# Kernel tuning notes

Measured on AMD Instinct MI355X. Metric: run time of the kernel, lower is better.

Reference implementation:

```python
import jax, jax.numpy as jnp
import numpy as np

CUTOFF = 2.0
LOG2 = float(np.log(2.0))

def ssp(x):
    # shifted softplus: softplus(x) - log(2)
    return jax.nn.softplus(x) - LOG2

def setup_inputs() -> dict:
    key = jax.random.key(0)
    ks = jax.random.split(key, 12)
    N, E, H, F, G = 10000, 320000, 256, 256, 50
    x = jax.random.normal(ks[0], (N, H), dtype=jnp.float32)
    edge_index = jax.random.randint(ks[1], (2, E), 0, N, dtype=jnp.int64)
    edge_weight = jax.random.normal(ks[2], (E, 3), dtype=jnp.float32)
    edge_attr = jax.random.normal(ks[3], (E, G), dtype=jnp.float32)
    s = lambda fan_in: 1.0 / np.sqrt(fan_in)
    mlp_w1 = jax.random.uniform(ks[4], (G, F), jnp.float32, -s(G), s(G))
    mlp_b1 = jax.random.uniform(ks[5], (F,), jnp.float32, -s(G), s(G))
    mlp_w2 = jax.random.uniform(ks[6], (F, F), jnp.float32, -s(F), s(F))
    mlp_b2 = jax.random.uniform(ks[7], (F,), jnp.float32, -s(F), s(F))
    lin1_w = jax.random.uniform(ks[8], (H, F), jnp.float32, -s(H), s(H))
    lin2_w = jax.random.uniform(ks[9], (F, H), jnp.float32, -s(F), s(F))
    lin2_b = jax.random.uniform(ks[10], (H,), jnp.float32, -s(F), s(F))
    return {"x": x, "edge_index": edge_index, "edge_weight": edge_weight,
            "edge_attr": edge_attr, "mlp_w1": mlp_w1, "mlp_b1": mlp_b1,
            "mlp_w2": mlp_w2, "mlp_b2": mlp_b2, "lin1_w": lin1_w,
            "lin2_w": lin2_w, "lin2_b": lin2_b}

def reference(x, edge_index, edge_weight, edge_attr,
              mlp_w1, mlp_b1, mlp_w2, mlp_b2, lin1_w, lin2_w, lin2_b):
    N = x.shape[0]
    # cutoff envelope on edge distances
    distances = jnp.linalg.norm(edge_weight, axis=1)                 # [E]
    C = 0.5 * (jnp.cos(distances * jnp.pi / CUTOFF) + 1.0)
    C = C * (distances <= CUTOFF)                                    # [E]
    # edge filter MLP
    W = ssp(edge_attr @ mlp_w1 + mlp_b1) @ mlp_w2 + mlp_b2           # [E, F]
    W = W * C[:, None]
    i, j = edge_index[0], edge_index[1]
    messages = W * (x[j] @ lin1_w)                                   # [E, F]
    agg = jax.ops.segment_sum(messages, i, num_segments=N)           # [N, F]
    h = ssp(agg @ lin2_w + lin2_b)                                   # [N, H]
    return x + h
```

## Files before the change

kernel.cpp:

```cpp
#include <hip/hip_runtime.h>
#include <hip/hip_bf16.h>
#include <stdint.h>

#define HF 256
#define GG 50

typedef __attribute__((ext_vector_type(8))) short bf16x8;
typedef __attribute__((ext_vector_type(4))) short bf16x4;
typedef __attribute__((ext_vector_type(4))) float f32x4;
typedef float f32x4a __attribute__((ext_vector_type(4), aligned(4)));

__device__ __forceinline__ uint32_t f2bf2u(float a, float b){
    __hip_bfloat162 h = __float22bfloat162_rn(make_float2(a, b));
    union { __hip_bfloat162 h; uint32_t u; } v; v.h = h; return v.u;
}
__device__ __forceinline__ float bf2f(short s){
    union { uint32_t u; float f; } v; v.u = ((uint32_t)(uint16_t)s) << 16;
    return v.f;
}
__device__ __forceinline__ float ssp_f(float x){
    float e = __builtin_amdgcn_exp2f(x * 1.44269504088896341f);
    return 0.69314718055994531f * __builtin_amdgcn_logf(1.0f + e)
         - 0.69314718055994531f;
}

__device__ __forceinline__ void pack_natural(const float* __restrict__ B,
                                             short* __restrict__ Bp,
                                             int idx, int KT, int kmax)
{
    int lane = idx & 63;
    int kt   = (idx >> 6) & (KT - 1);
    int ntg  = idx >> (6 + (KT == 2 ? 1 : 3));
    int col  = ntg * 16 + (lane & 15);
    int k0   = kt * 32 + (lane >> 4) * 8;
    uint32_t u[4];
#pragma unroll
    for (int jj = 0; jj < 4; ++jj) {
        int ka = k0 + 2*jj, kb = ka + 1;
        float a = (ka < kmax) ? B[(size_t)ka * HF + col] : 0.f;
        float b = (kb < kmax) ? B[(size_t)kb * HF + col] : 0.f;
        u[jj] = f2bf2u(a, b);
    }
    *(uint4*)&Bp[(size_t)idx * 8] = *(uint4*)u;
}

__global__ __launch_bounds__(256)
void prep_kernel(const float* __restrict__ w1, const float* __restrict__ b1,
                 const float* __restrict__ w2,
                 const float* __restrict__ lin1, const float* __restrict__ lin2,
                 short* __restrict__ w1p, short* __restrict__ w2p,
                 short* __restrict__ lin1p, short* __restrict__ lin2p,
                 const float* __restrict__ x, short* __restrict__ x_bf, int nx8,
                 const int* __restrict__ eidx, int* __restrict__ cnt, int E,
                 float* __restrict__ agg, int nAgg4, int gConv, int gHist)
{
    int b = blockIdx.x, tid = threadIdx.x;
    if (b < 8) {
        int idx  = b * 256 + tid;
        int lane = idx & 63;
        int kt   = (idx >> 6) & 1;
        int ntg  = idx >> 7;
        int col  = ntg * 16 + (lane & 15);
        int k0   = kt * 32 + (lane >> 4) * 8;
        uint32_t u[4];
#pragma unroll
        for (int jj = 0; jj < 4; ++jj) {
            int ka = k0 + 2*jj, kb = ka + 1;
            float va = (ka < GG) ? w1[(size_t)ka * HF + col]
                                 : ((ka == GG) ? b1[col] : 0.f);
            float vb = (kb < GG) ? w1[(size_t)kb * HF + col]
                                 : ((kb == GG) ? b1[col] : 0.f);
            u[jj] = f2bf2u(va, vb);
        }
        *(uint4*)&w1p[(size_t)idx * 8] = *(uint4*)u;
    } else if (b < 40) {
        int idx = (b - 8) * 256 + tid;
        int lane = idx & 63;
        int kt   = (idx >> 6) & 7;
        int ntg  = idx >> 9;
        int col  = ntg * 16 + (lane & 15);
        int s0   = kt * 32 + (lane >> 4) * 8;
        uint32_t u[4];
#pragma unroll
        for (int jj = 0; jj < 4; ++jj) {
            int sa = s0 + 2*jj, sb = sa + 1;
            int fa = (sa >> 6) * 64 + (sa & 3) * 16 + ((sa & 63) >> 2);
            int fb = (sb >> 6) * 64 + (sb & 3) * 16 + ((sb & 63) >> 2);
            u[jj] = f2bf2u(w2[(size_t)fa * HF + col], w2[(size_t)fb * HF + col]);
        }
        *(uint4*)&w2p[(size_t)idx * 8] = *(uint4*)u;
    } else if (b < 72) {
        pack_natural(lin1, lin1p, (b - 40) * 256 + tid, 8, HF);
    } else if (b < 104) {
        pack_natural(lin2, lin2p, (b - 72) * 256 + tid, 8, HF);
    } else if (b < 104 + gConv) {
        int idx = (b - 104) * 256 + tid;
        if (idx < nx8) {
            const float* xp = x + (size_t)idx * 8;
            float4 p0 = *(const float4*)(xp);
            float4 p1 = *(const float4*)(xp + 4);
            uint32_t u[4] = { f2bf2u(p0.x, p0.y), f2bf2u(p0.z, p0.w),
                              f2bf2u(p1.x, p1.y), f2bf2u(p1.z, p1.w) };
            *(uint4*)&x_bf[(size_t)idx * 8] = *(uint4*)u;
        }
    } else if (b < 104 + gConv + gHist) {
        int e = (b - 104 - gConv) * 256 + tid;
        if (e < E) atomicAdd(&cnt[eidx[e]], 1);
    } else {
        int idx = (b - 104 - gConv - gHist) * 256 + tid;
        if (idx < nAgg4) ((float4*)agg)[idx] = make_float4(0.f, 0.f, 0.f, 0.f);
    }
}

__global__ __launch_bounds__(256)
void gemm_scan_kernel(const short* __restrict__ x_bf, const short* __restrict__ lin1p,
                      short* __restrict__ y_p, int N,
                      const int* __restrict__ cnt, int* __restrict__ row,
                      int* __restrict__ cursor, int E, int gNode)
{
    const int tid = threadIdx.x;
    if ((int)blockIdx.x >= gNode) {
        __shared__ int part[256];
        const int CH = (N + 255) / 256;
        int lo = tid * CH;
        int hi = min(lo + CH, N);
        int s = 0;
        for (int n = lo; n < hi; ++n) s += cnt[n];
        part[tid] = s;
        __syncthreads();
        for (int off = 1; off < 256; off <<= 1) {
            int v = (tid >= off) ? part[tid - off] : 0;
            __syncthreads();
            part[tid] += v;
            __syncthreads();
        }
        int acc = part[tid] - s;
        for (int n = lo; n < hi; ++n) {
            row[n] = acc; cursor[n] = acc;
            acc += cnt[n];
        }
        if (tid == 255) row[N] = E;
        return;
    }
    const int lane = tid & 63;
    const int w    = tid >> 6;
    const int l15  = lane & 15;
    const int quad = lane >> 4;
    const int row0 = blockIdx.x * 32;

    f32x4 acc[2][4];
#pragma unroll
    for (int mt = 0; mt < 2; ++mt)
#pragma unroll
        for (int nt = 0; nt < 4; ++nt) acc[mt][nt] = (f32x4){0.f,0.f,0.f,0.f};

#pragma unroll 2
    for (int kt = 0; kt < 8; ++kt) {
        bf16x8 af[2];
#pragma unroll
        for (int mt = 0; mt < 2; ++mt) {
            int r = row0 + mt * 16 + l15;
            int rl = (r < N) ? r : 0;
            af[mt] = *(const bf16x8*)&x_bf[(size_t)rl * HF + kt * 32 + quad * 8];
        }
#pragma unroll
        for (int nt = 0; nt < 4; ++nt) {
            bf16x8 bfr = *(const bf16x8*)&lin1p[(size_t)(((w*4+nt)*8+kt)*64+lane)*8];
#pragma unroll
            for (int mt = 0; mt < 2; ++mt)
                acc[mt][nt] = __builtin_amdgcn_mfma_f32_16x16x32_bf16(af[mt], bfr, acc[mt][nt], 0, 0, 0);
        }
    }
#pragma unroll
    for (int mt = 0; mt < 2; ++mt) {
#pragma unroll
        for (int r = 0; r < 4; ++r) {
            int row_ = row0 + mt * 16 + quad * 4 + r;
            if (row_ < N) {
                uint2 u = make_uint2(f2bf2u(acc[mt][0][r], acc[mt][1][r]),
                                     f2bf2u(acc[mt][2][r], acc[mt][3][r]));
                *(uint2*)&y_p[(size_t)row_ * HF + w * 64 + l15 * 4] = u;
            }
        }
    }
}

__global__ __launch_bounds__(256)
void scatter_kernel(const int* __restrict__ eidx, int* __restrict__ cursor,
                    int* __restrict__ perm, int E)
{
    int e = blockIdx.x * 256 + threadIdx.x;
    if (e < E) {
        int pos = atomicAdd(&cursor[eidx[e]], 1);
        perm[pos] = e;
    }
}

__global__ __launch_bounds__(256)
void node2_kernel(const float* __restrict__ agg, const short* __restrict__ lin2p,
                  const float* __restrict__ bias, const float* __restrict__ x,
                  float* __restrict__ out, int N)
{
    const int tid  = threadIdx.x;
    const int lane = tid & 63;
    const int w    = tid >> 6;
    const int l15  = lane & 15;
    const int quad = lane >> 4;
    const int row0 = blockIdx.x * 32;

    f32x4 acc[2][4];
#pragma unroll
    for (int mt = 0; mt < 2; ++mt)
#pragma unroll
        for (int nt = 0; nt < 4; ++nt) acc[mt][nt] = (f32x4){0.f,0.f,0.f,0.f};

#pragma unroll 2
    for (int kt = 0; kt < 8; ++kt) {
        bf16x8 af[2];
#pragma unroll
        for (int mt = 0; mt < 2; ++mt) {
            int r = row0 + mt * 16 + l15;
            int rl = (r < N) ? r : 0;
            const float* ap = agg + (size_t)rl * HF + kt * 32 + quad * 8;
            float4 p0 = *(const float4*)(ap);
            float4 p1 = *(const float4*)(ap + 4);
            union { uint32_t u[4]; bf16x8 v; } c;
            c.u[0] = f2bf2u(p0.x, p0.y); c.u[1] = f2bf2u(p0.z, p0.w);
            c.u[2] = f2bf2u(p1.x, p1.y); c.u[3] = f2bf2u(p1.z, p1.w);
            af[mt] = c.v;
        }
#pragma unroll
        for (int nt = 0; nt < 4; ++nt) {
            bf16x8 bfr = *(const bf16x8*)&lin2p[(size_t)(((w*4+nt)*8+kt)*64+lane)*8];
#pragma unroll
            for (int mt = 0; mt < 2; ++mt)
                acc[mt][nt] = __builtin_amdgcn_mfma_f32_16x16x32_bf16(af[mt], bfr, acc[mt][nt], 0, 0, 0);
        }
    }
    float bs[4];
#pragma unroll
    for (int nt = 0; nt < 4; ++nt) bs[nt] = bias[w * 64 + nt * 16 + l15];
#pragma unroll
    for (int mt = 0; mt < 2; ++mt) {
#pragma unroll
        for (int r = 0; r < 4; ++r) {
            int row_ = row0 + mt * 16 + quad * 4 + r;
            if (row_ < N) {
#pragma unroll
                for (int nt = 0; nt < 4; ++nt) {
                    int f = w * 64 + nt * 16 + l15;
                    float v = ssp_f(acc[mt][nt][r] + bs[nt]) + x[(size_t)row_ * HF + f];
                    out[(size_t)row_ * HF + f] = v;
                }
            }
        }
    }
}

__global__ __launch_bounds__(256, 3)
void edge_mfma(const float* __restrict__ ea, const int* __restrict__ eidx,
               const float* __restrict__ ew,
               const short* __restrict__ w1p,
               const short* __restrict__ w2p, const float* __restrict__ b2,
               const short* __restrict__ y_p, const int* __restrict__ perm,
               const int* __restrict__ rowp,
               float* __restrict__ agg, int E)
{
    __shared__ short smem[19584];
    short* hid  = smem;
    short* msgT = smem;
    short* St   = smem + 18432;
    __shared__ int s_runnode[64];
    __shared__ unsigned char s_runcomp[64];

    const int tid  = threadIdx.x;
    const int lane = tid & 63;
    const int w    = tid >> 6;
    const int l15  = lane & 15;
    const int quad = lane >> 4;
    const int e0   = blockIdx.x * 64;

    int pp = e0 + lane;
    int eL = 0, iv = -1;
    float c = 0.f;
    if (pp < E) {
        eL = perm[pp];
        iv = eidx[eL];
        float d0 = ew[eL*3+0], d1 = ew[eL*3+1], d2 = ew[eL*3+2];
        float d = sqrtf(d0*d0 + d1*d1 + d2*d2);
        c = (d <= 2.0f) ? 0.5f * (__cosf(d * 1.57079632679489662f) + 1.0f) : 0.f;
    }
    int jv = eidx[E + eL];
    int ivn = __shfl_down(iv, 1);
    bool flag = (lane == 63) || (iv != ivn);
    unsigned long long bm = __ballot(flag);
    const int runcnt = (int)__popcll(bm);
    if (w == 0 && flag) {
        int rid = (int)__popcll(bm & ((1ull << lane) - 1ull));
        s_runnode[rid] = iv;
        int comp = 0;
        if (iv >= 0) {
            int lo = rowp[iv], hi = rowp[iv + 1];
            comp = (lo >= e0 && hi <= e0 + 64) ? 1 : 0;
        }
        s_runcomp[rid] = (unsigned char)comp;
    }

    bf16x8 a1[4][2];
#pragma unroll
    for (int mt = 0; mt < 4; ++mt) {
        int rp = __shfl(eL, mt * 16 + l15);
        const float* er = ea + (size_t)rp * GG;
        f32x4a p0 = *(const f32x4a*)(er + quad * 8);
        f32x4a p1 = *(const f32x4a*)(er + quad * 8 + 4);
        union { uint32_t u[4]; bf16x8 v; } ca;
        ca.u[0] = f2bf2u(p0[0], p0[1]); ca.u[1] = f2bf2u(p0[2], p0[3]);
        ca.u[2] = f2bf2u(p1[0], p1[1]); ca.u[3] = f2bf2u(p1[2], p1[3]);
        a1[mt][0] = ca.v;
        union { uint32_t u[4]; bf16x8 v; } cb;
        if (quad < 2) {
            f32x4a q0 = *(const f32x4a*)(er + 32 + quad * 8);
            f32x4a q1 = *(const f32x4a*)(er + 36 + quad * 8);
            cb.u[0] = f2bf2u(q0[0], q0[1]); cb.u[1] = f2bf2u(q0[2], q0[3]);
            cb.u[2] = f2bf2u(q1[0], q1[1]); cb.u[3] = f2bf2u(q1[2], q1[3]);
        } else if (quad == 2) {
            float2 q = *(const float2*)(er + 48);
            cb.u[0] = f2bf2u(q.x, q.y);
            cb.u[1] = 0x00003F80u;
            cb.u[2] = 0u; cb.u[3] = 0u;
        } else {
            cb.u[0] = 0u; cb.u[1] = 0u; cb.u[2] = 0u; cb.u[3] = 0u;
        }
        a1[mt][1] = cb.v;
    }

    f32x4 acc1[4][4];
#pragma unroll
    for (int mt = 0; mt < 4; ++mt)
#pragma unroll
        for (int nt = 0; nt < 4; ++nt) acc1[mt][nt] = (f32x4){0.f,0.f,0.f,0.f};
#pragma unroll
    for (int kt = 0; kt < 2; ++kt) {
#pragma unroll
        for (int nt = 0; nt < 4; ++nt) {
            bf16x8 bfr = *(const bf16x8*)&w1p[(size_t)(((w*4+nt)*2+kt)*64+lane)*8];
#pragma unroll
            for (int mt = 0; mt < 4; ++mt)
                acc1[mt][nt] = __builtin_amdgcn_mfma_f32_16x16x32_bf16(a1[mt][kt], bfr, acc1[mt][nt], 0, 0, 0);
        }
    }

    bf16x4 yv[4][4];
#pragma unroll
    for (int mt = 0; mt < 4; ++mt)
#pragma unroll
        for (int r = 0; r < 4; ++r) {
            int j = __shfl(jv, mt * 16 + quad * 4 + r);
            yv[mt][r] = *(const bf16x4*)&y_p[(size_t)j * HF + w * 64 + l15 * 4];
        }

#pragma unroll
    for (int mt = 0; mt < 4; ++mt) {
#pragma unroll
        for (int r = 0; r < 4; ++r) {
            int e = mt * 16 + quad * 4 + r;
            float v0 = ssp_f(acc1[mt][0][r]);
            float v1 = ssp_f(acc1[mt][1][r]);
            float v2 = ssp_f(acc1[mt][2][r]);
            float v3 = ssp_f(acc1[mt][3][r]);
            uint2 u = make_uint2(f2bf2u(v0, v1), f2bf2u(v2, v3));
            *(uint2*)&hid[e * 264 + w * 64 + l15 * 4] = u;
        }
    }
    __syncthreads();

    f32x4 acc2[4][4];
#pragma unroll
    for (int mt = 0; mt < 4; ++mt)
#pragma unroll
        for (int nt = 0; nt < 4; ++nt) acc2[mt][nt] = (f32x4){0.f,0.f,0.f,0.f};

#pragma unroll 2
    for (int kt = 0; kt < 8; ++kt) {
        bf16x8 af[4];
#pragma unroll
        for (int mt = 0; mt < 4; ++mt)
            af[mt] = *(bf16x8*)&hid[(mt * 16 + l15) * 264 + kt * 32 + quad * 8];
#pragma unroll
        for (int nt = 0; nt < 4; ++nt) {
            bf16x8 bfr = *(const bf16x8*)&w2p[(size_t)(((w*4+nt)*8+kt)*64+lane)*8];
#pragma unroll
            for (int mt = 0; mt < 4; ++mt)
                acc2[mt][nt] = __builtin_amdgcn_mfma_f32_16x16x32_bf16(af[mt], bfr, acc2[mt][nt], 0, 0, 0);
        }
    }
    __syncthreads();

    float bias2[4];
#pragma unroll
    for (int nt = 0; nt < 4; ++nt) bias2[nt] = b2[w * 64 + nt * 16 + l15];
    float cs[4][4];
#pragma unroll
    for (int mt = 0; mt < 4; ++mt)
#pragma unroll
        for (int r = 0; r < 4; ++r)
            cs[mt][r] = __shfl(c, mt * 16 + quad * 4 + r);
#pragma unroll
    for (int mt = 0; mt < 4; ++mt) {
#pragma unroll
        for (int nt = 0; nt < 4; ++nt) {
            int col = w * 64 + nt * 16 + l15;
            float v0 = (acc2[mt][nt][0] + bias2[nt]) * cs[mt][0] * bf2f(yv[mt][0][nt]);
            float v1 = (acc2[mt][nt][1] + bias2[nt]) * cs[mt][1] * bf2f(yv[mt][1][nt]);
            float v2 = (acc2[mt][nt][2] + bias2[nt]) * cs[mt][2] * bf2f(yv[mt][2][nt]);
            float v3 = (acc2[mt][nt][3] + bias2[nt]) * cs[mt][3] * bf2f(yv[mt][3][nt]);
            uint2 u = make_uint2(f2bf2u(v0, v1), f2bf2u(v2, v3));
            *(uint2*)&msgT[col * 72 + mt * 16 + quad * 4] = u;
        }
    }
    {
        int e   = tid & 63;
        int rb  = tid >> 6;
        int rid = (int)__popcll(bm & ((1ull << e) - 1ull));
#pragma unroll
        for (int q = 0; q < 4; ++q) {
            int r = rb + q * 4;
            St[r * 72 + e] = (rid == r) ? (short)0x3F80 : (short)0;
        }
    }
    __syncthreads();

    for (int ntg = 0; ntg * 16 < runcnt; ++ntg) {
        if (ntg > 0) {
            __syncthreads();
            int e   = tid & 63;
            int rb  = tid >> 6;
            int rid = (int)__popcll(bm & ((1ull << e) - 1ull));
#pragma unroll
            for (int q = 0; q < 4; ++q) {
                int r = rb + q * 4;
                St[r * 72 + e] = (rid == ntg * 16 + r) ? (short)0x3F80 : (short)0;
            }
            __syncthreads();
        }
        f32x4 acc3[4];
#pragma unroll
        for (int mt = 0; mt < 4; ++mt) acc3[mt] = (f32x4){0.f,0.f,0.f,0.f};
#pragma unroll
        for (int kt = 0; kt < 2; ++kt) {
            bf16x8 bS = *(bf16x8*)&St[l15 * 72 + kt * 32 + quad * 8];
#pragma unroll
            for (int mt = 0; mt < 4; ++mt) {
                bf16x8 af = *(bf16x8*)&msgT[(w*64 + mt*16 + l15) * 72 + kt*32 + quad*8];
                acc3[mt] = __builtin_amdgcn_mfma_f32_16x16x32_bf16(af, bS, acc3[mt], 0, 0, 0);
            }
        }
        int r = ntg * 16 + l15;
        if (r < runcnt) {
            int node = s_runnode[r];
            if (node >= 0) {
                float* ap = agg + (size_t)node * HF + w * 64 + quad * 4;
                if (s_runcomp[r]) {
#pragma unroll
                    for (int mt = 0; mt < 4; ++mt) {
                        float4 v = make_float4(acc3[mt][0], acc3[mt][1], acc3[mt][2], acc3[mt][3]);
                        *(float4*)(ap + mt * 16) = v;
                    }
                } else {
#pragma unroll
                    for (int mt = 0; mt < 4; ++mt)
#pragma unroll
                        for (int g = 0; g < 4; ++g)
                            atomicAdd(ap + mt * 16 + g, acc3[mt][g]);
                }
            }
        }
    }
}

extern "C" void kernel_launch(void* const* d_in, const int* in_sizes, int n_in,
                              void* d_out, int out_size, void* d_ws, size_t ws_size,
                              hipStream_t stream)
{
    const float* x     = (const float*)d_in[0];
    const int*   eidx  = (const int*)  d_in[1];
    const float* ew    = (const float*)d_in[2];
    const float* ea    = (const float*)d_in[3];
    const float* w1    = (const float*)d_in[4];
    const float* b1    = (const float*)d_in[5];
    const float* w2    = (const float*)d_in[6];
    const float* b2    = (const float*)d_in[7];
    const float* lin1  = (const float*)d_in[8];
    const float* lin2  = (const float*)d_in[9];
    const float* lin2b = (const float*)d_in[10];
    float* out = (float*)d_out;

    const int N = in_sizes[0] / HF;
    const int E = in_sizes[2] / 3;

    const size_t fN = (size_t)N * HF;
    float* agg    = (float*)d_ws;
    short* y_p    = (short*)(agg + fN);
    short* x_bf   = y_p + fN;
    int*   cnt    = (int*)(x_bf + fN);
    int*   row    = cnt + N;
    int*   cursor = row + (N + 8);
    int*   perm   = cursor + N;
    short* w1p    = (short*)(((uintptr_t)(perm + E) + 255) & ~(uintptr_t)255);
    short* w2p    = w1p + 16384;
    short* lin1p  = w2p + 65536;
    short* lin2p  = lin1p + 65536;

    hipMemsetAsync(cnt, 0, (size_t)N * sizeof(int), stream);

    const int nx8   = (int)(fN / 8);
    const int nAgg4 = (int)(fN / 4);
    const int gConv = (nx8 + 255) / 256;
    const int gHist = (E + 255) / 256;
    const int gZero = (nAgg4 + 255) / 256;
    prep_kernel<<<dim3(104 + gConv + gHist + gZero), dim3(256), 0, stream>>>(
        w1, b1, w2, lin1, lin2, w1p, w2p, lin1p, lin2p, x, x_bf, nx8,
        eidx, cnt, E, agg, nAgg4, gConv, gHist);

    const int gNode = (N + 31) / 32;
    gemm_scan_kernel<<<dim3(gNode + 1), dim3(256), 0, stream>>>(
        x_bf, lin1p, y_p, N, cnt, row, cursor, E, gNode);

    const int gScatter = (E + 255) / 256;
    scatter_kernel<<<dim3(gScatter), dim3(256), 0, stream>>>(eidx, cursor, perm, E);

    edge_mfma<<<dim3((E + 63) / 64), dim3(256), 0, stream>>>(
        ea, eidx, ew, w1p, w2p, b2, y_p, perm, row, agg, E);

    node2_kernel<<<dim3(gNode), dim3(256), 0, stream>>>(
        agg, lin2p, lin2b, x, out, N);
}
```

Measured before the change: 357.3 us.

## Make edge kernel persistent with register-resident weights and prefetch of next tile

Turns edge_mfma into a persistent grid-stride kernel capped at 1000 blocks. The W1 and W2 B-fragments and the bias are now loaded once into registers instead of being reloaded from global memory for every tile. The next tile's perm, edge index, distance, edge_attr and y gathers are issued during the current tile's compute to hide gather latency. The cost is a large rise in register pressure (w2f alone is 32 bf16x8 values per thread), which may cause spills or cut occupancy below the launch bound of 3, plus an extra barrier per iteration.

```diff
diff --git a/kernel.cpp b/kernel.cpp
--- a/kernel.cpp
+++ b/kernel.cpp
@@ -257,6 +257,65 @@
     }
 }
 
+__device__ __forceinline__ void issue_ea(const float* __restrict__ ea, int eLsrc,
+                                         int l15, int quad,
+                                         f32x4a (&rp0)[4], f32x4a (&rp1)[4],
+                                         f32x4a (&rq0)[4], f32x4a (&rq1)[4])
+{
+#pragma unroll
+    for (int mt = 0; mt < 4; ++mt) {
+        int rp = __shfl(eLsrc, mt * 16 + l15);
+        const float* er = ea + (size_t)rp * GG;
+        rp0[mt] = *(const f32x4a*)(er + quad * 8);
+        rp1[mt] = *(const f32x4a*)(er + quad * 8 + 4);
+        if (quad < 2) {
+            rq0[mt] = *(const f32x4a*)(er + 32 + quad * 8);
+            rq1[mt] = *(const f32x4a*)(er + 36 + quad * 8);
+        } else if (quad == 2) {
+            float2 q = *(const float2*)(er + 48);
+            rq0[mt][0] = q.x; rq0[mt][1] = q.y;
+        }
+    }
+}
+
+__device__ __forceinline__ void cvt_a1(int quad,
+                                       const f32x4a (&rp0)[4], const f32x4a (&rp1)[4],
+                                       const f32x4a (&rq0)[4], const f32x4a (&rq1)[4],
+                                       bf16x8 (&a1)[4][2])
+{
+#pragma unroll
+    for (int mt = 0; mt < 4; ++mt) {
+        union { uint32_t u[4]; bf16x8 v; } ca;
+        ca.u[0] = f2bf2u(rp0[mt][0], rp0[mt][1]); ca.u[1] = f2bf2u(rp0[mt][2], rp0[mt][3]);
+        ca.u[2] = f2bf2u(rp1[mt][0], rp1[mt][1]); ca.u[3] = f2bf2u(rp1[mt][2], rp1[mt][3]);
+        a1[mt][0] = ca.v;
+        union { uint32_t u[4]; bf16x8 v; } cb;
+        if (quad < 2) {
+            cb.u[0] = f2bf2u(rq0[mt][0], rq0[mt][1]); cb.u[1] = f2bf2u(rq0[mt][2], rq0[mt][3]);
+            cb.u[2] = f2bf2u(rq1[mt][0], rq1[mt][1]); cb.u[3] = f2bf2u(rq1[mt][2], rq1[mt][3]);
+        } else if (quad == 2) {
+            cb.u[0] = f2bf2u(rq0[mt][0], rq0[mt][1]);
+            cb.u[1] = 0x00003F80u;
+            cb.u[2] = 0u; cb.u[3] = 0u;
+        } else {
+            cb.u[0] = 0u; cb.u[1] = 0u; cb.u[2] = 0u; cb.u[3] = 0u;
+        }
+        a1[mt][1] = cb.v;
+    }
+}
+
+__device__ __forceinline__ void issue_yv(const short* __restrict__ y_p, int jvsrc,
+                                         int w, int l15, int quad, bf16x4 (&yv)[4][4])
+{
+#pragma unroll
+    for (int mt = 0; mt < 4; ++mt)
+#pragma unroll
+        for (int r = 0; r < 4; ++r) {
+            int j = __shfl(jvsrc, mt * 16 + quad * 4 + r);
+            yv[mt][r] = *(const bf16x4*)&y_p[(size_t)j * HF + w * 64 + l15 * 4];
+        }
+}
+
 __global__ __launch_bounds__(256, 3)
 void edge_mfma(const float* __restrict__ ea, const int* __restrict__ eidx,
                const float* __restrict__ ew,
@@ -264,7 +323,7 @@
                const short* __restrict__ w2p, const float* __restrict__ b2,
                const short* __restrict__ y_p, const int* __restrict__ perm,
                const int* __restrict__ rowp,
-               float* __restrict__ agg, int E)
+               float* __restrict__ agg, int E, int grid64)
 {
     __shared__ short smem[19584];
     short* hid  = smem;
@@ -278,8 +337,24 @@
     const int w    = tid >> 6;
     const int l15  = lane & 15;
     const int quad = lane >> 4;
-    const int e0   = blockIdx.x * 64;
-
+
+    bf16x8 w1f[2][4];
+#pragma unroll
+    for (int kt = 0; kt < 2; ++kt)
+#pragma unroll
+        for (int nt = 0; nt < 4; ++nt)
+            w1f[kt][nt] = *(const bf16x8*)&w1p[(size_t)(((w*4+nt)*2+kt)*64+lane)*8];
+    bf16x8 w2f[8][4];
+#pragma unroll
+    for (int kt = 0; kt < 8; ++kt)
+#pragma unroll
+        for (int nt = 0; nt < 4; ++nt)
+            w2f[kt][nt] = *(const bf16x8*)&w2p[(size_t)(((w*4+nt)*8+kt)*64+lane)*8];
+    float bias2[4];
+#pragma unroll
+    for (int nt = 0; nt < 4; ++nt) bias2[nt] = b2[w * 64 + nt * 16 + l15];
+
+    int e0 = blockIdx.x * 64;
     int pp = e0 + lane;
     int eL = 0, iv = -1;
     float c = 0.f;
@@ -291,190 +366,173 @@
         c = (d <= 2.0f) ? 0.5f * (__cosf(d * 1.57079632679489662f) + 1.0f) : 0.f;
     }
     int jv = eidx[E + eL];
-    int ivn = __shfl_down(iv, 1);
-    bool flag = (lane == 63) || (iv != ivn);
-    unsigned long long bm = __ballot(flag);
-    const int runcnt = (int)__popcll(bm);
-    if (w == 0 && flag) {
-        int rid = (int)__popcll(bm & ((1ull << lane) - 1ull));
-        s_runnode[rid] = iv;
-        int comp = 0;
-        if (iv >= 0) {
-            int lo = rowp[iv], hi = rowp[iv + 1];
-            comp = (lo >= e0 && hi <= e0 + 64) ? 1 : 0;
-        }
-        s_runcomp[rid] = (unsigned char)comp;
-    }
-
-    bf16x8 a1[4][2];
-#pragma unroll
-    for (int mt = 0; mt < 4; ++mt) {
-        int rp = __shfl(eL, mt * 16 + l15);
-        const float* er = ea + (size_t)rp * GG;
-        f32x4a p0 = *(const f32x4a*)(er + quad * 8);
-        f32x4a p1 = *(const f32x4a*)(er + quad * 8 + 4);
-        union { uint32_t u[4]; bf16x8 v; } ca;
-        ca.u[0] = f2bf2u(p0[0], p0[1]); ca.u[1] = f2bf2u(p0[2], p0[3]);
-        ca.u[2] = f2bf2u(p1[0], p1[1]); ca.u[3] = f2bf2u(p1[2], p1[3]);
-        a1[mt][0] = ca.v;
-        union { uint32_t u[4]; bf16x8 v; } cb;
-        if (quad < 2) {
-            f32x4a q0 = *(const f32x4a*)(er + 32 + quad * 8);
-            f32x4a q1 = *(const f32x4a*)(er + 36 + quad * 8);
-            cb.u[0] = f2bf2u(q0[0], q0[1]); cb.u[1] = f2bf2u(q0[2], q0[3]);
-            cb.u[2] = f2bf2u(q1[0], q1[1]); cb.u[3] = f2bf2u(q1[2], q1[3]);
-        } else if (quad == 2) {
-            float2 q = *(const float2*)(er + 48);
-            cb.u[0] = f2bf2u(q.x, q.y);
-            cb.u[1] = 0x00003F80u;
-            cb.u[2] = 0u; cb.u[3] = 0u;
-        } else {
-            cb.u[0] = 0u; cb.u[1] = 0u; cb.u[2] = 0u; cb.u[3] = 0u;
-        }
-        a1[mt][1] = cb.v;
-    }
-
-    f32x4 acc1[4][4];
-#pragma unroll
-    for (int mt = 0; mt < 4; ++mt)
-#pragma unroll
-        for (int nt = 0; nt < 4; ++nt) acc1[mt][nt] = (f32x4){0.f,0.f,0.f,0.f};
-#pragma unroll
-    for (int kt = 0; kt < 2; ++kt) {
-#pragma unroll
-        for (int nt = 0; nt < 4; ++nt) {
-            bf16x8 bfr = *(const bf16x8*)&w1p[(size_t)(((w*4+nt)*2+kt)*64+lane)*8];
-#pragma unroll
-            for (int mt = 0; mt < 4; ++mt)
-                acc1[mt][nt] = __builtin_amdgcn_mfma_f32_16x16x32_bf16(a1[mt][kt], bfr, acc1[mt][nt], 0, 0, 0);
-        }
-    }
-
+    f32x4a rp0[4], rp1[4], rq0[4], rq1[4];
+    issue_ea(ea, eL, l15, quad, rp0, rp1, rq0, rq1);
     bf16x4 yv[4][4];
-#pragma unroll
-    for (int mt = 0; mt < 4; ++mt)
-#pragma unroll
-        for (int r = 0; r < 4; ++r) {
-            int j = __shfl(jv, mt * 16 + quad * 4 + r);
-            yv[mt][r] = *(const bf16x4*)&y_p[(size_t)j * HF + w * 64 + l15 * 4];
-        }
-
-#pragma unroll
-    for (int mt = 0; mt < 4; ++mt) {
-#pragma unroll
-        for (int r = 0; r < 4; ++r) {
-            int e = mt * 16 + quad * 4 + r;
-            float v0 = ssp_f(acc1[mt][0][r]);
-            float v1 = ssp_f(acc1[mt][1][r]);
-            float v2 = ssp_f(acc1[mt][2][r]);
-            float v3 = ssp_f(acc1[mt][3][r]);
-            uint2 u = make_uint2(f2bf2u(v0, v1), f2bf2u(v2, v3));
-            *(uint2*)&hid[e * 264 + w * 64 + l15 * 4] = u;
-        }
-    }
-    __syncthreads();
-
-    f32x4 acc2[4][4];
-#pragma unroll
-    for (int mt = 0; mt < 4; ++mt)
-#pragma unroll
-        for (int nt = 0; nt < 4; ++nt) acc2[mt][nt] = (f32x4){0.f,0.f,0.f,0.f};
-
-#pragma unroll 2
-    for (int kt = 0; kt < 8; ++kt) {
-        bf16x8 af[4];
-#pragma unroll
-        for (int mt = 0; mt < 4; ++mt)
-            af[mt] = *(bf16x8*)&hid[(mt * 16 + l15) * 264 + kt * 32 + quad * 8];
-#pragma unroll
-        for (int nt = 0; nt < 4; ++nt) {
-            bf16x8 bfr = *(const bf16x8*)&w2p[(size_t)(((w*4+nt)*8+kt)*64+lane)*8];
-#pragma unroll
-            for (int mt = 0; mt < 4; ++mt)
-                acc2[mt][nt] = __builtin_amdgcn_mfma_f32_16x16x32_bf16(af[mt], bfr, acc2[mt][nt], 0, 0, 0);
-        }
-    }
-    __syncthreads();
-
-    float bias2[4];
-#pragma unroll
-    for (int nt = 0; nt < 4; ++nt) bias2[nt] = b2[w * 64 + nt * 16 + l15];
-    float cs[4][4];
-#pragma unroll
-    for (int mt = 0; mt < 4; ++mt)
-#pragma unroll
-        for (int r = 0; r < 4; ++r)
-            cs[mt][r] = __shfl(c, mt * 16 + quad * 4 + r);
-#pragma unroll
-    for (int mt = 0; mt < 4; ++mt) {
-#pragma unroll
-        for (int nt = 0; nt < 4; ++nt) {
-            int col = w * 64 + nt * 16 + l15;
-            float v0 = (acc2[mt][nt][0] + bias2[nt]) * cs[mt][0] * bf2f(yv[mt][0][nt]);
-            float v1 = (acc2[mt][nt][1] + bias2[nt]) * cs[mt][1] * bf2f(yv[mt][1][nt]);
-            float v2 = (acc2[mt][nt][2] + bias2[nt]) * cs[mt][2] * bf2f(yv[mt][2][nt]);
-            float v3 = (acc2[mt][nt][3] + bias2[nt]) * cs[mt][3] * bf2f(yv[mt][3][nt]);
-            uint2 u = make_uint2(f2bf2u(v0, v1), f2bf2u(v2, v3));
-            *(uint2*)&msgT[col * 72 + mt * 16 + quad * 4] = u;
-        }
-    }
-    {
-        int e   = tid & 63;
-        int rb  = tid >> 6;
-        int rid = (int)__popcll(bm & ((1ull << e) - 1ull));
-#pragma unroll
-        for (int q = 0; q < 4; ++q) {
-            int r = rb + q * 4;
-            St[r * 72 + e] = (rid == r) ? (short)0x3F80 : (short)0;
-        }
-    }
-    __syncthreads();
-
-    for (int ntg = 0; ntg * 16 < runcnt; ++ntg) {
-        if (ntg > 0) {
-            __syncthreads();
+    issue_yv(y_p, jv, w, l15, quad, yv);
+
+    for (; e0 < E; e0 += grid64) {
+        bf16x8 a1[4][2];
+        cvt_a1(quad, rp0, rp1, rq0, rq1, a1);
+
+        int ivn_ = __shfl_down(iv, 1);
+        bool flag = (lane == 63) || (iv != ivn_);
+        unsigned long long bm = __ballot(flag);
+        const int runcnt = (int)__popcll(bm);
+        if (w == 0 && flag) {
+            int rid = (int)__popcll(bm & ((1ull << lane) - 1ull));
+            s_runnode[rid] = iv;
+            int comp = 0;
+            if (iv >= 0) {
+                int lo = rowp[iv], hi = rowp[iv + 1];
+                comp = (lo >= e0 && hi <= e0 + 64) ? 1 : 0;
+            }
+            s_runcomp[rid] = (unsigned char)comp;
+        }
+        {
             int e   = tid & 63;
             int rb  = tid >> 6;
             int rid = (int)__popcll(bm & ((1ull << e) - 1ull));
 #pragma unroll
             for (int q = 0; q < 4; ++q) {
                 int r = rb + q * 4;
-                St[r * 72 + e] = (rid == ntg * 16 + r) ? (short)0x3F80 : (short)0;
-            }
-            __syncthreads();
-        }
-        f32x4 acc3[4];
-#pragma unroll
-        for (int mt = 0; mt < 4; ++mt) acc3[mt] = (f32x4){0.f,0.f,0.f,0.f};
-#pragma unroll
-        for (int kt = 0; kt < 2; ++kt) {
-            bf16x8 bS = *(bf16x8*)&St[l15 * 72 + kt * 32 + quad * 8];
-#pragma unroll
-            for (int mt = 0; mt < 4; ++mt) {
-                bf16x8 af = *(bf16x8*)&msgT[(w*64 + mt*16 + l15) * 72 + kt*32 + quad*8];
-                acc3[mt] = __builtin_amdgcn_mfma_f32_16x16x32_bf16(af, bS, acc3[mt], 0, 0, 0);
-            }
-        }
-        int r = ntg * 16 + l15;
-        if (r < runcnt) {
-            int node = s_runnode[r];
-            if (node >= 0) {
-                float* ap = agg + (size_t)node * HF + w * 64 + quad * 4;
-                if (s_runcomp[r]) {
-#pragma unroll
-                    for (int mt = 0; mt < 4; ++mt) {
-                        float4 v = make_float4(acc3[mt][0], acc3[mt][1], acc3[mt][2], acc3[mt][3]);
-                        *(float4*)(ap + mt * 16) = v;
+                St[r * 72 + e] = (rid == r) ? (short)0x3F80 : (short)0;
+            }
+        }
+
+        const int e0n = e0 + grid64;
+        const int ppn = e0n + lane;
+        int eLn = (ppn < E) ? perm[ppn] : 0;
+
+        f32x4 acc1[4][4];
+#pragma unroll
+        for (int mt = 0; mt < 4; ++mt)
+#pragma unroll
+            for (int nt = 0; nt < 4; ++nt) acc1[mt][nt] = (f32x4){0.f,0.f,0.f,0.f};
+#pragma unroll
+        for (int kt = 0; kt < 2; ++kt)
+#pragma unroll
+            for (int nt = 0; nt < 4; ++nt)
+#pragma unroll
+                for (int mt = 0; mt < 4; ++mt)
+                    acc1[mt][nt] = __builtin_amdgcn_mfma_f32_16x16x32_bf16(a1[mt][kt], w1f[kt][nt], acc1[mt][nt], 0, 0, 0);
+
+#pragma unroll
+        for (int mt = 0; mt < 4; ++mt) {
+#pragma unroll
+            for (int r = 0; r < 4; ++r) {
+                int e = mt * 16 + quad * 4 + r;
+                float v0 = ssp_f(acc1[mt][0][r]);
+                float v1 = ssp_f(acc1[mt][1][r]);
+                float v2 = ssp_f(acc1[mt][2][r]);
+                float v3 = ssp_f(acc1[mt][3][r]);
+                uint2 u = make_uint2(f2bf2u(v0, v1), f2bf2u(v2, v3));
+                *(uint2*)&hid[e * 264 + w * 64 + l15 * 4] = u;
+            }
+        }
+
+        int ivn = (ppn < E) ? eidx[eLn] : -1;
+        int jvn = eidx[E + eLn];
+        float d0n = ew[eLn*3+0], d1n = ew[eLn*3+1], d2n = ew[eLn*3+2];
+
+        __syncthreads();
+
+        f32x4 acc2[4][4];
+#pragma unroll
+        for (int mt = 0; mt < 4; ++mt)
+#pragma unroll
+            for (int nt = 0; nt < 4; ++nt) acc2[mt][nt] = (f32x4){0.f,0.f,0.f,0.f};
+#pragma unroll
+        for (int kt = 0; kt < 8; ++kt) {
+            bf16x8 af[4];
+#pragma unroll
+            for (int mt = 0; mt < 4; ++mt)
+                af[mt] = *(bf16x8*)&hid[(mt * 16 + l15) * 264 + kt * 32 + quad * 8];
+#pragma unroll
+            for (int nt = 0; nt < 4; ++nt)
+#pragma unroll
+                for (int mt = 0; mt < 4; ++mt)
+                    acc2[mt][nt] = __builtin_amdgcn_mfma_f32_16x16x32_bf16(af[mt], w2f[kt][nt], acc2[mt][nt], 0, 0, 0);
+        }
+        __syncthreads();
+
+        float cs[4][4];
+#pragma unroll
+        for (int mt = 0; mt < 4; ++mt)
+#pragma unroll
+            for (int r = 0; r < 4; ++r)
+                cs[mt][r] = __shfl(c, mt * 16 + quad * 4 + r);
+#pragma unroll
+        for (int mt = 0; mt < 4; ++mt) {
+#pragma unroll
+            for (int nt = 0; nt < 4; ++nt) {
+                int col = w * 64 + nt * 16 + l15;
+                float v0 = (acc2[mt][nt][0] + bias2[nt]) * cs[mt][0] * bf2f(yv[mt][0][nt]);
+                float v1 = (acc2[mt][nt][1] + bias2[nt]) * cs[mt][1] * bf2f(yv[mt][1][nt]);
+                float v2 = (acc2[mt][nt][2] + bias2[nt]) * cs[mt][2] * bf2f(yv[mt][2][nt]);
+                float v3 = (acc2[mt][nt][3] + bias2[nt]) * cs[mt][3] * bf2f(yv[mt][3][nt]);
+                uint2 u = make_uint2(f2bf2u(v0, v1), f2bf2u(v2, v3));
+                *(uint2*)&msgT[col * 72 + mt * 16 + quad * 4] = u;
+            }
+        }
+
+        float dn = sqrtf(d0n*d0n + d1n*d1n + d2n*d2n);
+        float cn = (ppn < E && dn <= 2.0f)
+                 ? 0.5f * (__cosf(dn * 1.57079632679489662f) + 1.0f) : 0.f;
+        issue_yv(y_p, jvn, w, l15, quad, yv);
+
+        for (int ntg = 0; ntg * 16 < runcnt; ++ntg) {
+            if (ntg > 0) {
+                __syncthreads();
+                int e   = tid & 63;
+                int rb  = tid >> 6;
+                int rid = (int)__popcll(bm & ((1ull << e) - 1ull));
+#pragma unroll
+                for (int q = 0; q < 4; ++q) {
+                    int r = rb + q * 4;
+                    St[r * 72 + e] = (rid == ntg * 16 + r) ? (short)0x3F80 : (short)0;
+                }
+                __syncthreads();
+            }
+            f32x4 acc3[4];
+#pragma unroll
+            for (int mt = 0; mt < 4; ++mt) acc3[mt] = (f32x4){0.f,0.f,0.f,0.f};
+#pragma unroll
+            for (int kt = 0; kt < 2; ++kt) {
+                bf16x8 bS = *(bf16x8*)&St[l15 * 72 + kt * 32 + quad * 8];
+#pragma unroll
+                for (int mt = 0; mt < 4; ++mt) {
+                    bf16x8 af = *(bf16x8*)&msgT[(w*64 + mt*16 + l15) * 72 + kt*32 + quad*8];
+                    acc3[mt] = __builtin_amdgcn_mfma_f32_16x16x32_bf16(af, bS, acc3[mt], 0, 0, 0);
+                }
+            }
+            int r = ntg * 16 + l15;
+            if (r < runcnt) {
+                int node = s_runnode[r];
+                if (node >= 0) {
+                    float* ap = agg + (size_t)node * HF + w * 64 + quad * 4;
+                    if (s_runcomp[r]) {
+#pragma unroll
+                        for (int mt = 0; mt < 4; ++mt) {
+                            float4 v = make_float4(acc3[mt][0], acc3[mt][1], acc3[mt][2], acc3[mt][3]);
+                            *(float4*)(ap + mt * 16) = v;
+                        }
+                    } else {
+#pragma unroll
+                        for (int mt = 0; mt < 4; ++mt)
+#pragma unroll
+                            for (int g = 0; g < 4; ++g)
+                                atomicAdd(ap + mt * 16 + g, acc3[mt][g]);
                     }
-                } else {
-#pragma unroll
-                    for (int mt = 0; mt < 4; ++mt)
-#pragma unroll
-                        for (int g = 0; g < 4; ++g)
-                            atomicAdd(ap + mt * 16 + g, acc3[mt][g]);
                 }
             }
         }
+
+        issue_ea(ea, eLn, l15, quad, rp0, rp1, rq0, rq1);
+
+        __syncthreads();
+
+        eL = eLn; iv = ivn; jv = jvn; c = cn;
     }
 }
 
@@ -529,8 +587,10 @@
     const int gScatter = (E + 255) / 256;
     scatter_kernel<<<dim3(gScatter), dim3(256), 0, stream>>>(eidx, cursor, perm, E);
 
-    edge_mfma<<<dim3((E + 63) / 64), dim3(256), 0, stream>>>(
-        ea, eidx, ew, w1p, w2p, b2, y_p, perm, row, agg, E);
+    const int nT = (E + 63) / 64;
+    const int gE = nT < 1000 ? nT : 1000;
+    edge_mfma<<<dim3(gE), dim3(256), 0, stream>>>(
+        ea, eidx, ew, w1p, w2p, b2, y_p, perm, row, agg, E, gE * 64);
 
     node2_kernel<<<dim3(gNode), dim3(256), 0, stream>>>(
         agg, lin2p, lin2b, x, out, N);
```

Result: slower. 654.5 us (+83.2%).
